# Performance work log

Measured on AMD Instinct MI355X. Metric: run time of the kernel, lower is better.

The kernel has to match this reference:

```python
import jax, jax.numpy as jnp
import numpy as np

IN_CHANNELS = 512
NUM_HEADS = 8
HEAD_CH = IN_CHANNELS // NUM_HEADS


def setup_inputs() -> dict:
    key = jax.random.key(0)
    k0, k1, k2, k3, k4 = jax.random.split(key, 5)
    B, C, H, W = 4, IN_CHANNELS, 128, 128
    x = jax.random.normal(k0, (B, C, H, W), dtype=jnp.float32)
    # 1x1 Conv2d weights == per-pixel linear layers over channels
    s_in = 1.0 / np.sqrt(C)
    Wqkv = jax.random.uniform(k1, (3 * C, C), dtype=jnp.float32, minval=-s_in, maxval=s_in)
    bqkv = jax.random.uniform(k2, (3 * C,), dtype=jnp.float32, minval=-s_in, maxval=s_in)
    Wout = jax.random.uniform(k3, (C, C), dtype=jnp.float32, minval=-s_in, maxval=s_in)
    bout = jax.random.uniform(k4, (C,), dtype=jnp.float32, minval=-s_in, maxval=s_in)
    return {"x": x, "Wqkv": Wqkv, "bqkv": bqkv, "Wout": Wout, "bout": bout}


def _axial_attention(x, Wqkv, bqkv, Wout, bout):
    B, C, H, W = x.shape
    nh, d = NUM_HEADS, HEAD_CH
    scale = 1.0 / jnp.sqrt(jnp.asarray(d, dtype=x.dtype))

    # 1x1 conv qkv projection: [B, 3C, H, W]
    qkv = jnp.einsum('bchw,oc->bohw', x, Wqkv) + bqkv[None, :, None, None]
    q, k, v = jnp.split(qkv, 3, axis=1)
    # [B, nh, d, H, W]
    q = q.reshape(B, nh, d, H, W)
    k = k.reshape(B, nh, d, H, W)
    v = v.reshape(B, nh, d, H, W)

    # Row attention: for each row h, attend across width (w over u)
    scores_row = jnp.einsum('bndhw,bndhu->bnhwu', q, k) * scale  # [B,nh,H,W,W]
    probs_row = jax.nn.softmax(scores_row, axis=-1)
    out_row = jnp.einsum('bnhwu,bndhu->bndhw', probs_row, v)  # [B,nh,d,H,W]

    # Column attention: for each column w, attend across height (h over g)
    scores_col = jnp.einsum('bndhw,bndgw->bnwhg', q, k) * scale  # [B,nh,W,H,H]
    probs_col = jax.nn.softmax(scores_col, axis=-1)
    out_col = jnp.einsum('bnwhg,bndgw->bndhw', probs_col, v)  # [B,nh,d,H,W]

    out = (out_row + out_col).reshape(B, C, H, W)
    # 1x1 conv output projection
    return jnp.einsum('bchw,oc->bohw', out, Wout) + bout[None, :, None, None]


def reference(x, Wqkv, bqkv, Wout, bout):
    return _axial_attention(x, Wqkv, bqkv, Wout, bout)
```

## Files before the change

kernel.cpp:

```cpp
#include <hip/hip_runtime.h>

#define DI __device__ __forceinline__

typedef __attribute__((ext_vector_type(4))) float f32x4;
typedef __attribute__((ext_vector_type(8))) short s16x8;
typedef __attribute__((ext_vector_type(4))) short s16x4;
typedef unsigned short u16;

#define AS_G(p) ((const __attribute__((address_space(1))) void*)(p))
#define AS_L(p) ((__attribute__((address_space(3))) void*)(p))

DI short f2bf(float f) {
  union { float f; unsigned u; } v; v.f = f;
  unsigned r = v.u + 0x7FFFu + ((v.u >> 16) & 1u);
  return (short)(r >> 16);
}
DI float bf2f(short h) {
  union { unsigned u; float f; } v; v.u = ((unsigned)(u16)h) << 16; return v.f;
}

#define MFMA(a, b, c) __builtin_amdgcn_mfma_f32_16x16x32_bf16((a), (b), (c), 0, 0, 0)

__global__ void cast_weights_kernel(const float* __restrict__ wqkv, u16* __restrict__ wqkv_bf,
                                    const float* __restrict__ wout, u16* __restrict__ wout_bf) {
  const int n1 = 1536 * 512 / 4, n2 = 512 * 512 / 4;
  for (int c = blockIdx.x * blockDim.x + threadIdx.x; c < n1 + n2; c += gridDim.x * blockDim.x) {
    const float4* src; u16* dst; int idx;
    if (c < n1) { src = (const float4*)wqkv; dst = wqkv_bf; idx = c; }
    else        { src = (const float4*)wout; dst = wout_bf; idx = c - n1; }
    float4 v = src[idx];
    s16x4 o;
    o[0] = f2bf(v.x); o[1] = f2bf(v.y); o[2] = f2bf(v.z); o[3] = f2bf(v.w);
    *(s16x4*)(dst + (long)idx * 4) = o;
  }
}

template<bool IN_F32>
__global__ __launch_bounds__(256)
void transpose_kernel(const void* __restrict__ in, u16* __restrict__ out,
                      int in_rstride, int out_rstride, long plane_in, long plane_out) {
  __shared__ __align__(16) u16 t[64][72];
  const int tid = threadIdx.x;
  const long bi = (long)blockIdx.z * plane_in;
  const long bo = (long)blockIdx.z * plane_out;
  const int r0 = blockIdx.y * 64, c0 = blockIdx.x * 64;
#pragma unroll
  for (int i = 0; i < 4; ++i) {
    int c = tid + i * 256;
    int row = c >> 4, c4 = c & 15;
    s16x4 pk;
    if (IN_F32) {
      const float4 v = *(const float4*)((const float*)in + bi + (long)(r0 + row) * in_rstride + c0 + c4 * 4);
      pk[0] = f2bf(v.x); pk[1] = f2bf(v.y); pk[2] = f2bf(v.z); pk[3] = f2bf(v.w);
    } else {
      pk = *(const s16x4*)((const u16*)in + bi + (long)(r0 + row) * in_rstride + c0 + c4 * 4);
    }
    *(s16x4*)&t[row][c4 * 4] = pk;
  }
  __syncthreads();
#pragma unroll
  for (int i = 0; i < 2; ++i) {
    int c = tid + i * 256;
    int orow = c >> 3, u = c & 7;
    s16x8 pk;
#pragma unroll
    for (int j = 0; j < 8; ++j) pk[j] = (short)t[u * 8 + j][orow];
    *(s16x8*)(out + bo + (long)(c0 + orow) * out_rstride + r0 + u * 8) = pk;
  }
}

template<int EPI>
__global__ __launch_bounds__(256, 2)
void gemm_kernel(const u16* __restrict__ A, const u16* __restrict__ B,
                 const float* __restrict__ bias,
                 u16* __restrict__ out_qk, u16* __restrict__ out_v,
                 float* __restrict__ out_f) {
  __shared__ __align__(16) u16 As[128 * 64];
  __shared__ __align__(16) u16 Bs[128 * 64];
  const int tid = threadIdx.x;
  const int lane = tid & 63, wid = tid >> 6;
  const int l15 = lane & 15, g4 = lane >> 4;
  const int wr = wid >> 1, wc = wid & 1;
  const int m0 = blockIdx.y * 128, n0 = blockIdx.x * 128;
  const int z = blockIdx.z;
  const u16* Bp = B + (long)z * 8388608;

  f32x4 acc[4][4];
#pragma unroll
  for (int i = 0; i < 4; ++i)
#pragma unroll
    for (int j = 0; j < 4; ++j) { f32x4 z4 = {0.f, 0.f, 0.f, 0.f}; acc[i][j] = z4; }

  const int srow = wid * 32 + (lane >> 3);
  const int su = lane & 7;
  auto stage = [&](int kt) {
#pragma unroll
    for (int i = 0; i < 4; ++i) {
      int row = srow + i * 8;
      int ksw = (su ^ (row & 7)) * 8;
      __builtin_amdgcn_global_load_lds(AS_G(A + (long)(m0 + row) * 512 + kt * 64 + ksw),
                                       AS_L(As + wid * 2048 + i * 512), 16, 0, 0);
    }
#pragma unroll
    for (int i = 0; i < 4; ++i) {
      int row = srow + i * 8;
      int ksw = (su ^ (row & 7)) * 8;
      __builtin_amdgcn_global_load_lds(AS_G(Bp + (long)(n0 + row) * 512 + kt * 64 + ksw),
                                       AS_L(Bs + wid * 2048 + i * 512), 16, 0, 0);
    }
  };

  for (int kt = 0; kt < 8; ++kt) {
    __syncthreads();
    stage(kt);
    __syncthreads();
#pragma unroll
    for (int ks = 0; ks < 2; ++ks) {
      s16x8 af[4], bfr[4];
#pragma unroll
      for (int mi = 0; mi < 4; ++mi) {
        int row = (wr * 4 + mi) * 16 + l15;
        af[mi] = *(const s16x8*)(As + row * 64 + (((ks * 4 + g4) ^ (row & 7)) * 8));
      }
#pragma unroll
      for (int ni = 0; ni < 4; ++ni) {
        int row = (wc * 4 + ni) * 16 + l15;
        bfr[ni] = *(const s16x8*)(Bs + row * 64 + (((ks * 4 + g4) ^ (row & 7)) * 8));
      }
#pragma unroll
      for (int mi = 0; mi < 4; ++mi)
#pragma unroll
        for (int ni = 0; ni < 4; ++ni)
          acc[mi][ni] = MFMA(af[mi], bfr[ni], acc[mi][ni]);
    }
  }

  if (EPI == 0) {
    u16* qk_b = out_qk + (long)z * 16777216;
    u16* v_b  = out_v + (long)z * 8388608;
    if (m0 < 1024) {
#pragma unroll
      for (int mi = 0; mi < 4; ++mi) {
        int o0 = m0 + (wr * 4 + mi) * 16 + 4 * g4;
        float b0 = bias[o0], b1 = bias[o0 + 1], b2 = bias[o0 + 2], b3 = bias[o0 + 3];
#pragma unroll
        for (int ni = 0; ni < 4; ++ni) {
          int p = n0 + (wc * 4 + ni) * 16 + l15;
          s16x4 pk;
          pk[0] = f2bf(acc[mi][ni][0] + b0);
          pk[1] = f2bf(acc[mi][ni][1] + b1);
          pk[2] = f2bf(acc[mi][ni][2] + b2);
          pk[3] = f2bf(acc[mi][ni][3] + b3);
          *(s16x4*)(qk_b + (long)p * 1024 + o0) = pk;
        }
      }
    } else {
#pragma unroll
      for (int mi = 0; mi < 4; ++mi) {
        int o0 = m0 + (wr * 4 + mi) * 16 + 4 * g4;
#pragma unroll
        for (int ni = 0; ni < 4; ++ni) {
          int p = n0 + (wc * 4 + ni) * 16 + l15;
#pragma unroll
          for (int r = 0; r < 4; ++r)
            v_b[(long)(o0 - 1024 + r) * 16384 + p] = (u16)f2bf(acc[mi][ni][r] + bias[o0 + r]);
        }
      }
    }
  } else {
    float* of = out_f + (long)z * 8388608;
#pragma unroll
    for (int mi = 0; mi < 4; ++mi) {
      int o0 = m0 + (wr * 4 + mi) * 16 + 4 * g4;
#pragma unroll
      for (int ni = 0; ni < 4; ++ni) {
        int p = n0 + (wc * 4 + ni) * 16 + l15;
#pragma unroll
        for (int r = 0; r < 4; ++r)
          of[(long)(o0 + r) * 16384 + p] = acc[mi][ni][r] + bias[o0 + r];
      }
    }
  }
}

template<int MODE>
__global__ __launch_bounds__(512, 2)
void attn_kernel(const u16* __restrict__ qk_t_g, const u16* __restrict__ vsrc_g,
                 u16* __restrict__ outp_g) {
  __shared__ __align__(16) u16 smem[24576];
  u16* qT = smem;
  u16* kT = smem + 8192;
  u16* vS = smem + 16384;
  u16* P  = smem;

  const int tid = threadIdx.x;
  const int lane = tid & 63, wid = tid >> 6;
  const int l15 = lane & 15, g4 = lane >> 4;
  const int b = blockIdx.x >> 10;
  const int gidx = blockIdx.x & 1023;
  const int n = gidx >> 7, pos = gidx & 127;

  const u16* qk_t = qk_t_g + (long)b * 16777216;
  const u16* vsrc = vsrc_g + (long)b * 8388608;
  u16* outp = outp_g + (long)b * 8388608;

  long q_base, q_rstride;
  if (MODE == 0) { q_base = (long)pos * 128 * 1024 + n * 64; q_rstride = 1024; }
  else           { q_base = (long)pos * 1024 + n * 64;       q_rstride = 128 * 1024; }
  const long v_base = (long)n * 64 * 16384 + (long)pos * 128;

#pragma unroll
  for (int j = 0; j < 6; ++j) {
    int t = wid + j * 8;
    if (t < 32) {
      int which = t >> 4;
      int tt = t & 15;
      int row = tt * 8 + (lane >> 3);
      int u = lane & 7;
      const u16* src = qk_t + q_base + which * 512 + (long)row * q_rstride + ((u ^ (row & 7)) * 8);
      __builtin_amdgcn_global_load_lds(AS_G(src), AS_L(smem + t * 512), 16, 0, 0);
    } else {
      int tt = t - 32;
      int row = tt * 4 + (lane >> 4);
      int u = lane & 15;
      const u16* src = vsrc + v_base + (long)row * 16384 + ((u ^ (row & 15)) * 8);
      __builtin_amdgcn_global_load_lds(AS_G(src), AS_L(smem + t * 512), 16, 0, 0);
    }
  }
  __syncthreads();

  f32x4 acc[8];
#pragma unroll
  for (int nt = 0; nt < 8; ++nt) { f32x4 z = {0.f, 0.f, 0.f, 0.f}; acc[nt] = z; }
  s16x8 aq[2];
  {
    int row = wid * 16 + l15;
#pragma unroll
    for (int ks = 0; ks < 2; ++ks)
      aq[ks] = *(const s16x8*)(qT + row * 64 + (((ks * 4 + g4) ^ (row & 7)) * 8));
  }
#pragma unroll
  for (int nt = 0; nt < 8; ++nt) {
    int rowk = nt * 16 + l15;
#pragma unroll
    for (int ks = 0; ks < 2; ++ks) {
      s16x8 bk = *(const s16x8*)(kT + rowk * 64 + (((ks * 4 + g4) ^ (rowk & 7)) * 8));
      acc[nt] = MFMA(aq[ks], bk, acc[nt]);
    }
  }

#pragma unroll
  for (int r = 0; r < 4; ++r) {
    float m = -1e30f;
#pragma unroll
    for (int nt = 0; nt < 8; ++nt) m = fmaxf(m, acc[nt][r]);
    m = fmaxf(m, __shfl_xor(m, 1));
    m = fmaxf(m, __shfl_xor(m, 2));
    m = fmaxf(m, __shfl_xor(m, 4));
    m = fmaxf(m, __shfl_xor(m, 8));
    float s = 0.f;
#pragma unroll
    for (int nt = 0; nt < 8; ++nt) {
      float e = __expf((acc[nt][r] - m) * 0.125f);
      acc[nt][r] = e; s += e;
    }
    s += __shfl_xor(s, 1); s += __shfl_xor(s, 2);
    s += __shfl_xor(s, 4); s += __shfl_xor(s, 8);
    float rinv = 1.0f / s;
#pragma unroll
    for (int nt = 0; nt < 8; ++nt) acc[nt][r] *= rinv;
  }
  __syncthreads();

#pragma unroll
  for (int nt = 0; nt < 8; ++nt) {
    int u = nt * 16 + l15;
#pragma unroll
    for (int r = 0; r < 4; ++r) {
      int w = wid * 16 + 4 * g4 + r;
      int ch = (u >> 3) ^ (w & 15);
      P[w * 128 + ch * 8 + (u & 7)] = (u16)f2bf(acc[nt][r]);
    }
  }
  __syncthreads();

  const int mw = wid >> 2, nw = wid & 3;
  f32x4 pacc[2][2];
#pragma unroll
  for (int mi = 0; mi < 2; ++mi)
#pragma unroll
    for (int ni = 0; ni < 2; ++ni) { f32x4 z = {0.f, 0.f, 0.f, 0.f}; pacc[mi][ni] = z; }
#pragma unroll
  for (int ks = 0; ks < 4; ++ks) {
    s16x8 av[2], bp[2];
#pragma unroll
    for (int mi = 0; mi < 2; ++mi) {
      int d = (mw * 2 + mi) * 16 + l15;
      av[mi] = *(const s16x8*)(vS + d * 128 + (((ks * 4 + g4) ^ (d & 15)) * 8));
    }
#pragma unroll
    for (int ni = 0; ni < 2; ++ni) {
      int w = (nw * 2 + ni) * 16 + l15;
      bp[ni] = *(const s16x8*)(P + w * 128 + (((ks * 4 + g4) ^ (w & 15)) * 8));
    }
#pragma unroll
    for (int mi = 0; mi < 2; ++mi)
#pragma unroll
      for (int ni = 0; ni < 2; ++ni)
        pacc[mi][ni] = MFMA(av[mi], bp[ni], pacc[mi][ni]);
  }

  long out_pbase, out_pstr;
  if (MODE == 0) { out_pbase = (long)pos * 128 * 512; out_pstr = 512; }
  else           { out_pbase = (long)pos * 512;       out_pstr = 128 * 512; }
#pragma unroll
  for (int mi = 0; mi < 2; ++mi) {
    int d0 = (mw * 2 + mi) * 16 + 4 * g4;
#pragma unroll
    for (int ni = 0; ni < 2; ++ni) {
      int nj = (nw * 2 + ni) * 16 + l15;
      long base = out_pbase + (long)nj * out_pstr + n * 64 + d0;
      if (MODE == 0) {
        s16x4 pk;
#pragma unroll
        for (int r = 0; r < 4; ++r) pk[r] = f2bf(pacc[mi][ni][r]);
        *(s16x4*)(outp + base) = pk;
      } else {
        s16x4 old = *(const s16x4*)(outp + base);
        s16x4 pk;
#pragma unroll
        for (int r = 0; r < 4; ++r) pk[r] = f2bf(bf2f(old[r]) + pacc[mi][ni][r]);
        *(s16x4*)(outp + base) = pk;
      }
    }
  }
}

extern "C" void kernel_launch(void* const* d_in, const int* in_sizes, int n_in,
                              void* d_out, int out_size, void* d_ws, size_t ws_size,
                              hipStream_t stream) {
  const float* x    = (const float*)d_in[0];
  const float* wqkv = (const float*)d_in[1];
  const float* bqkv = (const float*)d_in[2];
  const float* wout = (const float*)d_in[3];
  const float* bout = (const float*)d_in[4];
  float* out = (float*)d_out;

  char* ws = (char*)d_ws;
  size_t off = 0;
  auto alloc = [&](size_t bytes) { void* p = ws + off; off += (bytes + 255) & ~(size_t)255; return p; };
  u16* wqkv_bf = (u16*)alloc(1536L * 512 * 2);
  u16* wout_bf = (u16*)alloc(512L * 512 * 2);
  u16* xT      = (u16*)alloc(4L * 16384 * 512 * 2);
  u16* qk_t    = (u16*)alloc(4L * 16384 * 1024 * 2);
  u16* v_buf   = (u16*)alloc(4L * 512 * 16384 * 2);
  u16* vT      = (u16*)alloc(4L * 512 * 16384 * 2);
  u16* attn_T  = (u16*)alloc(4L * 16384 * 512 * 2);

  cast_weights_kernel<<<256, 256, 0, stream>>>(wqkv, wqkv_bf, wout, wout_bf);
  transpose_kernel<true><<<dim3(256, 8, 4), 256, 0, stream>>>(
      x, xT, 16384, 512, 512L * 16384, 16384L * 512);
  gemm_kernel<0><<<dim3(128, 12, 4), 256, 0, stream>>>(wqkv_bf, xT, bqkv, qk_t, v_buf, nullptr);
  transpose_kernel<false><<<dim3(2, 2, 2048), 256, 0, stream>>>(v_buf, vT, 128, 128, 16384, 16384);
  attn_kernel<0><<<dim3(4096), 512, 0, stream>>>(qk_t, v_buf, attn_T);
  attn_kernel<1><<<dim3(4096), 512, 0, stream>>>(qk_t, vT, attn_T);
  gemm_kernel<1><<<dim3(128, 4, 4), 256, 0, stream>>>(wout_bf, attn_T, bout, nullptr, nullptr, out);
}
```

Baseline: 391.1 us.

## Double-buffer GEMM LDS tiles and stage epilogue through LDS for coalesced stores

The GEMM main loop now uses two LDS buffers. The next K-tile is issued with global_load_lds while the MFMAs run on the current tile, which drops one barrier per iteration. All epilogues (QK, V and the f32 output projection) first write results into a padded LDS tile, then write to global memory with 16-byte row-contiguous vector stores. The old epilogue did strided scalar stores. The cost is double the LDS per block (64KB) plus extra barriers and LDS traffic in the epilogue.

```diff
diff --git a/kernel.cpp b/kernel.cpp
--- a/kernel.cpp
+++ b/kernel.cpp
@@ -75,8 +75,7 @@
                  const float* __restrict__ bias,
                  u16* __restrict__ out_qk, u16* __restrict__ out_v,
                  float* __restrict__ out_f) {
-  __shared__ __align__(16) u16 As[128 * 64];
-  __shared__ __align__(16) u16 Bs[128 * 64];
+  __shared__ __align__(16) u16 sAB[2][16384];
   const int tid = threadIdx.x;
   const int lane = tid & 63, wid = tid >> 6;
   const int l15 = lane & 15, g4 = lane >> 4;
@@ -93,7 +92,9 @@
 
   const int srow = wid * 32 + (lane >> 3);
   const int su = lane & 7;
-  auto stage = [&](int kt) {
+  auto stage = [&](int kt, int buf) {
+    u16* As = sAB[buf];
+    u16* Bs = sAB[buf] + 8192;
 #pragma unroll
     for (int i = 0; i < 4; ++i) {
       int row = srow + i * 8;
@@ -110,10 +111,13 @@
     }
   };
 
+  stage(0, 0);
+  __syncthreads();
+  int cur = 0;
   for (int kt = 0; kt < 8; ++kt) {
-    __syncthreads();
-    stage(kt);
-    __syncthreads();
+    if (kt < 7) stage(kt + 1, cur ^ 1);
+    const u16* As = sAB[cur];
+    const u16* Bs = sAB[cur] + 8192;
 #pragma unroll
     for (int ks = 0; ks < 2; ++ks) {
       s16x8 af[4], bfr[4];
@@ -133,7 +137,12 @@
         for (int ni = 0; ni < 4; ++ni)
           acc[mi][ni] = MFMA(af[mi], bfr[ni], acc[mi][ni]);
     }
-  }
+    __syncthreads();
+    cur ^= 1;
+  }
+
+  u16* tile = (u16*)sAB;
+  float* tilef = (float*)sAB;
 
   if (EPI == 0) {
     u16* qk_b = out_qk + (long)z * 16777216;
@@ -141,43 +150,84 @@
     if (m0 < 1024) {
 #pragma unroll
       for (int mi = 0; mi < 4; ++mi) {
-        int o0 = m0 + (wr * 4 + mi) * 16 + 4 * g4;
+        int ol = (wr * 4 + mi) * 16 + 4 * g4;
+        int o0 = m0 + ol;
         float b0 = bias[o0], b1 = bias[o0 + 1], b2 = bias[o0 + 2], b3 = bias[o0 + 3];
 #pragma unroll
         for (int ni = 0; ni < 4; ++ni) {
-          int p = n0 + (wc * 4 + ni) * 16 + l15;
+          int pl = (wc * 4 + ni) * 16 + l15;
           s16x4 pk;
           pk[0] = f2bf(acc[mi][ni][0] + b0);
           pk[1] = f2bf(acc[mi][ni][1] + b1);
           pk[2] = f2bf(acc[mi][ni][2] + b2);
           pk[3] = f2bf(acc[mi][ni][3] + b3);
-          *(s16x4*)(qk_b + (long)p * 1024 + o0) = pk;
+          *(s16x4*)(tile + pl * 136 + ol) = pk;
         }
       }
+      __syncthreads();
+#pragma unroll
+      for (int i = 0; i < 8; ++i) {
+        int row = i * 16 + (tid >> 4);
+        int c8 = (tid & 15) * 8;
+        s16x8 vr = *(const s16x8*)(tile + row * 136 + c8);
+        *(s16x8*)(qk_b + (long)(n0 + row) * 1024 + m0 + c8) = vr;
+      }
     } else {
 #pragma unroll
       for (int mi = 0; mi < 4; ++mi) {
-        int o0 = m0 + (wr * 4 + mi) * 16 + 4 * g4;
+        int cl = (wr * 4 + mi) * 16 + 4 * g4;
+        int o0 = m0 + cl;
 #pragma unroll
         for (int ni = 0; ni < 4; ++ni) {
-          int p = n0 + (wc * 4 + ni) * 16 + l15;
+          int pl = (wc * 4 + ni) * 16 + l15;
 #pragma unroll
           for (int r = 0; r < 4; ++r)
-            v_b[(long)(o0 - 1024 + r) * 16384 + p] = (u16)f2bf(acc[mi][ni][r] + bias[o0 + r]);
+            tile[(cl + r) * 136 + pl] = (u16)f2bf(acc[mi][ni][r] + bias[o0 + r]);
         }
+      }
+      __syncthreads();
+#pragma unroll
+      for (int i = 0; i < 8; ++i) {
+        int row = i * 16 + (tid >> 4);
+        int c8 = (tid & 15) * 8;
+        s16x8 vr = *(const s16x8*)(tile + row * 136 + c8);
+        *(s16x8*)(v_b + (long)(m0 - 1024 + row) * 16384 + n0 + c8) = vr;
       }
     }
   } else {
     float* of = out_f + (long)z * 8388608;
 #pragma unroll
-    for (int mi = 0; mi < 4; ++mi) {
-      int o0 = m0 + (wr * 4 + mi) * 16 + 4 * g4;
-#pragma unroll
-      for (int ni = 0; ni < 4; ++ni) {
-        int p = n0 + (wc * 4 + ni) * 16 + l15;
-#pragma unroll
-        for (int r = 0; r < 4; ++r)
-          of[(long)(o0 + r) * 16384 + p] = acc[mi][ni][r] + bias[o0 + r];
+    for (int pass = 0; pass < 2; ++pass) {
+      if (pass) __syncthreads();
+#pragma unroll
+      for (int mi2 = 0; mi2 < 2; ++mi2) {
+        int mi = pass * 2 + mi2;
+        int ol = mi2 * 16 + 4 * g4 + ((wr & 1) ? 64 : 0);
+        (void)ol;
+      }
+      if (wr == pass) {
+#pragma unroll
+        for (int mi = 0; mi < 4; ++mi) {
+          int ol = (wr * 4 + mi) * 16 + 4 * g4;
+          int o0 = m0 + ol;
+          float b0 = bias[o0], b1 = bias[o0 + 1], b2 = bias[o0 + 2], b3 = bias[o0 + 3];
+          float bb[4] = {b0, b1, b2, b3};
+#pragma unroll
+          for (int ni = 0; ni < 4; ++ni) {
+            int pl = (wc * 4 + ni) * 16 + l15;
+#pragma unroll
+            for (int r = 0; r < 4; ++r)
+              tilef[(ol - pass * 64 + r) * 136 + pl] = acc[mi][ni][r] + bb[r];
+          }
+        }
+      }
+      __syncthreads();
+#pragma unroll
+      for (int i = 0; i < 8; ++i) {
+        int row = i * 8 + (tid >> 5);
+        int c4 = (tid & 31) * 4;
+        f32x4 vr = *(const f32x4*)(tilef + row * 136 + c4);
+        *(f32x4*)(of + (long)(m0 + pass * 64 + row) * 16384 + n0 + c4) = vr;
       }
     }
   }
@@ -231,7 +281,7 @@
 
   f32x4 acc[8];
 #pragma unroll
-  for (int nt = 0; nt < 8; ++nt) { f32x4 z = {0.f, 0.f, 0.f, 0.f}; acc[nt] = z; }
+  for (int nt = 0; nt < 8; ++nt) { f32x4 zz = {0.f, 0.f, 0.f, 0.f}; acc[nt] = zz; }
   s16x8 aq[2];
   {
     int row = wid * 16 + l15;
@@ -289,7 +339,7 @@
 #pragma unroll
   for (int mi = 0; mi < 2; ++mi)
 #pragma unroll
-    for (int ni = 0; ni < 2; ++ni) { f32x4 z = {0.f, 0.f, 0.f, 0.f}; pacc[mi][ni] = z; }
+    for (int ni = 0; ni < 2; ++ni) { f32x4 zz = {0.f, 0.f, 0.f, 0.f}; pacc[mi][ni] = zz; }
 #pragma unroll
   for (int ks = 0; ks < 4; ++ks) {
     s16x8 av[2], bp[2];
```

Result: no change. 387.0 us (-1.0%).
